# Performance work log

Hardware: AMD Instinct MI355X
Metric: run time of the kernel (lower is better)

## Reference

```python
import jax, jax.numpy as jnp
import numpy as np

U, I = 100000, 50000
N = U + I
NNZ = 3200000
EMB = 64
N_LAYERS = 3
LAYER_CL = 1
EPS = 0.1
BN_EPS = 1e-5
LRELU_SLOPE = 0.01


def setup_inputs() -> dict:
    key = jax.random.key(0)
    ks = jax.random.split(key, 8)
    user_emb = jax.random.normal(ks[0], (U, EMB), jnp.float32) * 0.1
    item_emb = jax.random.normal(ks[1], (I, EMB), jnp.float32) * 0.1
    adj_rows = jnp.sort(jax.random.randint(ks[2], (NNZ,), 0, N, jnp.int32))
    adj_cols = jax.random.randint(ks[3], (NNZ,), 0, N, jnp.int32)
    # symmetric-normalized adjacency values ~ 1/deg scale
    adj_vals = jax.random.uniform(ks[4], (NNZ,), jnp.float32) * 0.05
    Wu = jax.random.normal(ks[5], (EMB, EMB), jnp.float32) / jnp.sqrt(EMB)
    Wi = jax.random.normal(ks[6], (EMB, EMB), jnp.float32) / jnp.sqrt(EMB)
    zeros = jnp.zeros((EMB,), jnp.float32)
    ones = jnp.ones((EMB,), jnp.float32)
    return {
        'user_emb': user_emb, 'item_emb': item_emb,
        'adj_rows': adj_rows, 'adj_cols': adj_cols, 'adj_vals': adj_vals,
        'Wu': Wu, 'bu': zeros, 'gu': ones, 'btu': zeros,
        'Wi': Wi, 'bi': zeros, 'gi': ones, 'bti': zeros,
    }


def _noise_gen(x, W, b, g, bt):
    # Linear -> LeakyReLU -> BatchNorm1d(train-mode batch stats, dropout omitted) -> L2 normalize
    h = x @ W.T + b
    h = jnp.where(h >= 0, h, LRELU_SLOPE * h)
    mu = jnp.mean(h, axis=0)
    var = jnp.mean(jnp.square(h - mu), axis=0)  # biased var, as BatchNorm1d
    h = (h - mu) * jax.lax.rsqrt(var + BN_EPS) * g + bt
    nrm = jnp.maximum(jnp.linalg.norm(h, axis=-1, keepdims=True), 1e-12)
    return h / nrm


def _spmm(rows, cols, vals, x):
    # out[r] += vals_e * x[cols_e]  -> sparse @ dense
    return jax.ops.segment_sum(vals[:, None] * x[cols], rows, num_segments=N)


def reference(user_emb, item_emb, adj_rows, adj_cols, adj_vals,
              Wu, bu, gu, btu, Wi, bi, gi, bti):
    ego = jnp.concatenate([user_emb, item_emb], axis=0)  # [N, EMB]
    emb_cl = ego
    acc = jnp.zeros_like(ego)
    for k in range(N_LAYERS):
        ego = _spmm(adj_rows, adj_cols, adj_vals, ego)
        # perturbed=True path: distribution-aware noise injection
        noise_u = _noise_gen(ego[:U], Wu, bu, gu, btu)
        noise_i = _noise_gen(ego[U:], Wi, bi, gi, bti)
        noise = jnp.concatenate([noise_u, noise_i], axis=0)
        ego = ego + jnp.sign(ego) * noise * EPS
        acc = acc + ego
        if k == LAYER_CL - 1:
            emb_cl = ego
    final = acc / N_LAYERS  # mean over layers
    return (final[:U], final[U:], emb_cl[:U], emb_cl[U:])
```

## Files before the change

kernel.cpp:

```cpp
#include <hip/hip_runtime.h>

#define U_CNT 100000
#define I_CNT 50000
#define N_CNT 150000
#define NNZ_CNT 3200000
#define EMB 64


__global__ void init_ego_kernel(const float* __restrict__ ue, const float* __restrict__ ie,
                                float* __restrict__ ego) {
  const int total = N_CNT * EMB, ucnt = U_CNT * EMB;
  for (int i = blockIdx.x * blockDim.x + threadIdx.x; i < total; i += gridDim.x * blockDim.x)
    ego[i] = (i < ucnt) ? ue[i] : ie[i - ucnt];
}

__global__ void build_row_ptr_kernel(const int* __restrict__ rows, int* __restrict__ rp) {
  int r = blockIdx.x * blockDim.x + threadIdx.x;
  if (r > N_CNT) return;
  int lo = 0, hi = NNZ_CNT;
  while (lo < hi) { int mid = (lo + hi) >> 1; if (rows[mid] < r) lo = mid + 1; else hi = mid; }
  rp[r] = lo;
}

__global__ void zero_stats_kernel(double* __restrict__ stats) {
  stats[threadIdx.x] = 0.0;
}

__global__ __launch_bounds__(256) void spmm_kernel(const float* __restrict__ x, float* __restrict__ y,
                            const int* __restrict__ rp, const int* __restrict__ cols,
                            const float* __restrict__ vals) {
  const int wave = threadIdx.x >> 6, lane = threadIdx.x & 63;
  const int row = blockIdx.x * 4 + wave;
  if (row >= N_CNT) return;
  const int e0 = rp[row], e1 = rp[row + 1];
  float acc = 0.f;
  int e = e0;
  const int nmain = e0 + ((e1 - e0) & ~7);
  for (; e < nmain; e += 8) {
    float xv[8], vv[8];
    #pragma unroll
    for (int j = 0; j < 8; ++j) {
      const int c = cols[e + j];
      vv[j] = vals[e + j];
      xv[j] = x[(size_t)c * EMB + lane];
    }
    #pragma unroll
    for (int j = 0; j < 8; ++j)
      acc = __fadd_rn(acc, __fmul_rn(vv[j], xv[j]));
  }
  for (; e < e1; ++e) {
    const int c = cols[e];
    acc = __fadd_rn(acc, __fmul_rn(vals[e], x[(size_t)c * EMB + lane]));
  }
  y[(size_t)row * EMB + lane] = acc;
}

#define GU 512
#define GI 256
__global__ __launch_bounds__(256) void gemv_stats_kernel(const float* __restrict__ y, double* __restrict__ h,
                                  const float* __restrict__ Wu, const float* __restrict__ bu,
                                  const float* __restrict__ Wi, const float* __restrict__ bi,
                                  double* __restrict__ stats) {
  __shared__ float ysh[4][EMB];
  __shared__ double red[4][EMB];
  const int wave = threadIdx.x >> 6, lane = threadIdx.x & 63;
  const bool isU = blockIdx.x < GU;
  const int blk = isU ? blockIdx.x : blockIdx.x - GU;
  const int nblk = isU ? GU : GI;
  const int nrows = isU ? U_CNT : I_CNT;
  const float* Wf = isU ? Wu : Wi;
  const float* bf = isU ? bu : bi;
  const float* yp = isU ? y : (y + (size_t)U_CNT * EMB);
  double* hp = isU ? h : (h + (size_t)U_CNT * EMB);
  double* sum_out = stats + (isU ? 0 : 128);
  double* sq_out = sum_out + 64;

  float w[EMB];
  #pragma unroll
  for (int k = 0; k < EMB; k += 4) {
    float4 t = *(const float4*)&Wf[lane * EMB + k];
    w[k] = t.x; w[k+1] = t.y; w[k+2] = t.z; w[k+3] = t.w;
  }
  const double bj = (double)bf[lane];
  double s = 0.0, q = 0.0;
  for (int r = blk * 4 + wave; r < nrows; r += nblk * 4) {
    ysh[wave][lane] = yp[(size_t)r * EMB + lane];
    double acc = 0.0;
    #pragma unroll
    for (int k = 0; k < EMB; ++k) acc = fma((double)ysh[wave][k], (double)w[k], acc);
    double h0 = acc + bj;
    h0 = (h0 >= 0.0) ? h0 : 0.01 * h0;
    hp[(size_t)r * EMB + lane] = h0;
    s += h0;
    q = fma(h0, h0, q);
  }
  red[wave][lane] = s;
  __syncthreads();
  if (wave == 0)
    atomicAdd(&sum_out[lane], red[0][lane] + red[1][lane] + red[2][lane] + red[3][lane]);
  __syncthreads();
  red[wave][lane] = q;
  __syncthreads();
  if (wave == 0)
    atomicAdd(&sq_out[lane], red[0][lane] + red[1][lane] + red[2][lane] + red[3][lane]);
}

__global__ void finalize_stats_kernel(const double* __restrict__ stats, double* __restrict__ muR) {
  const int t = threadIdx.x;
  if (t >= 128) return;
  const int lane = t & 63;
  const bool isU = t < 64;
  const double* sp = stats + (isU ? 0 : 128);
  const double cnt = isU ? (double)U_CNT : (double)I_CNT;
  const double mu = sp[lane] / cnt;
  double var = sp[64 + lane] / cnt - mu * mu;
  if (var < 0.0) var = 0.0;
  muR[t] = mu;
  muR[128 + t] = 1.0 / sqrt(var + 1e-5);
}

__global__ __launch_bounds__(256) void apply_kernel(const float* __restrict__ y, const double* __restrict__ h,
                             float* __restrict__ ego, float* __restrict__ out_final,
                             float* __restrict__ out_cl,
                             const double* __restrict__ muR,
                             const float* __restrict__ gu, const float* __restrict__ btu,
                             const float* __restrict__ gi, const float* __restrict__ bti,
                             int layer) {
  const int wave = threadIdx.x >> 6, lane = threadIdx.x & 63;
  const bool isU = blockIdx.x < GU;
  const int blk = isU ? blockIdx.x : blockIdx.x - GU;
  const int nblk = isU ? GU : GI;
  const int nrows = isU ? U_CNT : I_CNT;
  const size_t off = isU ? 0 : (size_t)U_CNT * EMB;
  const double muj = muR[(isU ? 0 : 64) + lane];
  const double Rj = muR[128 + (isU ? 0 : 64) + lane];
  const double gj = (double)(isU ? gu[lane] : gi[lane]);
  const double btj = (double)(isU ? btu[lane] : bti[lane]);
  for (int r = blk * 4 + wave; r < nrows; r += nblk * 4) {
    const size_t o = off + (size_t)r * EMB + lane;
    const float yv = y[o];
    const double hv = h[o];
    const double hn = ((hv - muj) * Rj) * gj + btj;
    double ss = hn * hn;
    #pragma unroll
    for (int sh = 32; sh > 0; sh >>= 1) ss += __shfl_xor(ss, sh, 64);
    double nrm = sqrt(ss);
    if (nrm < 1e-12) nrm = 1e-12;
    const float noise = (float)(hn / nrm);
    const float sgn = (yv > 0.f) ? 1.f : ((yv < 0.f) ? -1.f : 0.f);
    const float t2 = __fmul_rn(__fmul_rn(sgn, noise), 0.1f);
    const float en = __fadd_rn(yv, t2);
    ego[o] = en;
    if (layer == 0) { out_final[o] = en; out_cl[o] = en; }
    else if (layer == 1) { out_final[o] = __fadd_rn(out_final[o], en); }
    else { out_final[o] = __fdiv_rn(__fadd_rn(out_final[o], en), 3.0f); }
  }
}

extern "C" void kernel_launch(void* const* d_in, const int* in_sizes, int n_in,
                              void* d_out, int out_size, void* d_ws, size_t ws_size,
                              hipStream_t stream) {
  const float* user_emb = (const float*)d_in[0];
  const float* item_emb = (const float*)d_in[1];
  const int* adj_rows = (const int*)d_in[2];
  const int* adj_cols = (const int*)d_in[3];
  const float* adj_vals = (const float*)d_in[4];
  const float* Wu = (const float*)d_in[5];
  const float* bu = (const float*)d_in[6];
  const float* gu = (const float*)d_in[7];
  const float* btu = (const float*)d_in[8];
  const float* Wi = (const float*)d_in[9];
  const float* bi = (const float*)d_in[10];
  const float* gi = (const float*)d_in[11];
  const float* bti = (const float*)d_in[12];
  float* out = (float*)d_out;

  float* ego = (float*)d_ws;
  float* y = ego + (size_t)N_CNT * EMB;
  double* h = (double*)(y + (size_t)N_CNT * EMB);
  double* stats = h + (size_t)N_CNT * EMB;
  double* muR = stats + 256;
  int* rp = (int*)(muR + 256);

  float* out_final = out;
  float* out_cl = out + (size_t)N_CNT * EMB;

  init_ego_kernel<<<2048, 256, 0, stream>>>(user_emb, item_emb, ego);
  build_row_ptr_kernel<<<(N_CNT + 1 + 255) / 256, 256, 0, stream>>>(adj_rows, rp);

  for (int layer = 0; layer < 3; ++layer) {
    zero_stats_kernel<<<1, 256, 0, stream>>>(stats);
    spmm_kernel<<<(N_CNT + 3) / 4, 256, 0, stream>>>(ego, y, rp, adj_cols, adj_vals);
    gemv_stats_kernel<<<GU + GI, 256, 0, stream>>>(y, h, Wu, bu, Wi, bi, stats);
    finalize_stats_kernel<<<1, 128, 0, stream>>>(stats, muR);
    apply_kernel<<<GU + GI, 256, 0, stream>>>(y, h, ego, out_final, out_cl, muR,
                                              gu, btu, gi, bti, layer);
  }
}
```

Baseline: 783.7 us.

## Recompute linear layer in apply kernel instead of storing double h buffer

```diff
diff --git a/kernel.cpp b/kernel.cpp
--- a/kernel.cpp
+++ b/kernel.cpp
@@ -24,6 +24,7 @@
 
 __global__ void zero_stats_kernel(double* __restrict__ stats) {
   stats[threadIdx.x] = 0.0;
+  stats[256 + threadIdx.x] = 0.0;
 }
 
 __global__ __launch_bounds__(256) void spmm_kernel(const float* __restrict__ x, float* __restrict__ y,
@@ -57,7 +58,8 @@
 
 #define GU 512
 #define GI 256
-__global__ __launch_bounds__(256) void gemv_stats_kernel(const float* __restrict__ y, double* __restrict__ h,
+
+__global__ __launch_bounds__(256) void stats_kernel(const float* __restrict__ y,
                                   const float* __restrict__ Wu, const float* __restrict__ bu,
                                   const float* __restrict__ Wi, const float* __restrict__ bi,
                                   double* __restrict__ stats) {
@@ -71,7 +73,6 @@
   const float* Wf = isU ? Wu : Wi;
   const float* bf = isU ? bu : bi;
   const float* yp = isU ? y : (y + (size_t)U_CNT * EMB);
-  double* hp = isU ? h : (h + (size_t)U_CNT * EMB);
   double* sum_out = stats + (isU ? 0 : 128);
   double* sq_out = sum_out + 64;
 
@@ -90,7 +91,6 @@
     for (int k = 0; k < EMB; ++k) acc = fma((double)ysh[wave][k], (double)w[k], acc);
     double h0 = acc + bj;
     h0 = (h0 >= 0.0) ? h0 : 0.01 * h0;
-    hp[(size_t)r * EMB + lane] = h0;
     s += h0;
     q = fma(h0, h0, q);
   }
@@ -105,42 +105,53 @@
     atomicAdd(&sq_out[lane], red[0][lane] + red[1][lane] + red[2][lane] + red[3][lane]);
 }
 
-__global__ void finalize_stats_kernel(const double* __restrict__ stats, double* __restrict__ muR) {
-  const int t = threadIdx.x;
-  if (t >= 128) return;
-  const int lane = t & 63;
-  const bool isU = t < 64;
-  const double* sp = stats + (isU ? 0 : 128);
-  const double cnt = isU ? (double)U_CNT : (double)I_CNT;
-  const double mu = sp[lane] / cnt;
-  double var = sp[64 + lane] / cnt - mu * mu;
-  if (var < 0.0) var = 0.0;
-  muR[t] = mu;
-  muR[128 + t] = 1.0 / sqrt(var + 1e-5);
-}
-
-__global__ __launch_bounds__(256) void apply_kernel(const float* __restrict__ y, const double* __restrict__ h,
+__global__ __launch_bounds__(256) void apply_kernel(const float* __restrict__ y,
                              float* __restrict__ ego, float* __restrict__ out_final,
                              float* __restrict__ out_cl,
-                             const double* __restrict__ muR,
+                             const double* __restrict__ stats, double* __restrict__ stats_next,
+                             const float* __restrict__ Wu, const float* __restrict__ bu,
                              const float* __restrict__ gu, const float* __restrict__ btu,
+                             const float* __restrict__ Wi, const float* __restrict__ bi,
                              const float* __restrict__ gi, const float* __restrict__ bti,
                              int layer) {
+  __shared__ float ysh[4][EMB];
   const int wave = threadIdx.x >> 6, lane = threadIdx.x & 63;
+  if (blockIdx.x == 0) stats_next[threadIdx.x] = 0.0;
   const bool isU = blockIdx.x < GU;
   const int blk = isU ? blockIdx.x : blockIdx.x - GU;
   const int nblk = isU ? GU : GI;
   const int nrows = isU ? U_CNT : I_CNT;
   const size_t off = isU ? 0 : (size_t)U_CNT * EMB;
-  const double muj = muR[(isU ? 0 : 64) + lane];
-  const double Rj = muR[128 + (isU ? 0 : 64) + lane];
+  const float* Wf = isU ? Wu : Wi;
+  const float* bf = isU ? bu : bi;
+
+  float w[EMB];
+  #pragma unroll
+  for (int k = 0; k < EMB; k += 4) {
+    float4 t = *(const float4*)&Wf[lane * EMB + k];
+    w[k] = t.x; w[k+1] = t.y; w[k+2] = t.z; w[k+3] = t.w;
+  }
+  const double bj = (double)bf[lane];
+  const double cnt = isU ? (double)U_CNT : (double)I_CNT;
+  const double S = stats[(isU ? 0 : 128) + lane];
+  const double Q = stats[(isU ? 0 : 128) + 64 + lane];
+  const double muj = S / cnt;
+  double var = Q / cnt - muj * muj;
+  if (var < 0.0) var = 0.0;
+  const double Rj = 1.0 / sqrt(var + 1e-5);
   const double gj = (double)(isU ? gu[lane] : gi[lane]);
   const double btj = (double)(isU ? btu[lane] : bti[lane]);
+
   for (int r = blk * 4 + wave; r < nrows; r += nblk * 4) {
     const size_t o = off + (size_t)r * EMB + lane;
     const float yv = y[o];
-    const double hv = h[o];
-    const double hn = ((hv - muj) * Rj) * gj + btj;
+    ysh[wave][lane] = yv;
+    double acc = 0.0;
+    #pragma unroll
+    for (int k = 0; k < EMB; ++k) acc = fma((double)ysh[wave][k], (double)w[k], acc);
+    double h0 = acc + bj;
+    h0 = (h0 >= 0.0) ? h0 : 0.01 * h0;
+    const double hn = ((h0 - muj) * Rj) * gj + btj;
     double ss = hn * hn;
     #pragma unroll
     for (int sh = 32; sh > 0; sh >>= 1) ss += __shfl_xor(ss, sh, 64);
@@ -177,23 +188,23 @@
 
   float* ego = (float*)d_ws;
   float* y = ego + (size_t)N_CNT * EMB;
-  double* h = (double*)(y + (size_t)N_CNT * EMB);
-  double* stats = h + (size_t)N_CNT * EMB;
-  double* muR = stats + 256;
-  int* rp = (int*)(muR + 256);
+  double* stats = (double*)(y + (size_t)N_CNT * EMB);
+  int* rp = (int*)(stats + 512);
 
   float* out_final = out;
   float* out_cl = out + (size_t)N_CNT * EMB;
 
   init_ego_kernel<<<2048, 256, 0, stream>>>(user_emb, item_emb, ego);
   build_row_ptr_kernel<<<(N_CNT + 1 + 255) / 256, 256, 0, stream>>>(adj_rows, rp);
+  zero_stats_kernel<<<1, 256, 0, stream>>>(stats);
 
   for (int layer = 0; layer < 3; ++layer) {
-    zero_stats_kernel<<<1, 256, 0, stream>>>(stats);
+    double* stats_cur = stats + (layer & 1) * 256;
+    double* stats_next = stats + ((layer + 1) & 1) * 256;
     spmm_kernel<<<(N_CNT + 3) / 4, 256, 0, stream>>>(ego, y, rp, adj_cols, adj_vals);
-    gemv_stats_kernel<<<GU + GI, 256, 0, stream>>>(y, h, Wu, bu, Wi, bi, stats);
-    finalize_stats_kernel<<<1, 128, 0, stream>>>(stats, muR);
-    apply_kernel<<<GU + GI, 256, 0, stream>>>(y, h, ego, out_final, out_cl, muR,
-                                              gu, btu, gi, bti, layer);
-  }
-}
+    stats_kernel<<<GU + GI, 256, 0, stream>>>(y, Wu, bu, Wi, bi, stats_cur);
+    apply_kernel<<<GU + GI, 256, 0, stream>>>(y, ego, out_final, out_cl,
+                                              stats_cur, stats_next,
+                                              Wu, bu, gu, btu, Wi, bi, gi, bti, layer);
+  }
+}
```

After: 1.045 ms. +33.3%, slower.
